# Optimization experiments

Hardware: AMD Instinct MI355X
Metric: run time of the kernel (lower is better)

The kernel has to match this reference:

```python
import jax, jax.numpy as jnp
import numpy as np

B, S_X, S_Y = 2, 2048, 2048
C1, C2, H, D, W_EXP = 1024, 1024, 16, 64, 4
EPS = 1e-5


def _layernorm(x, w, b):
    mu = jnp.mean(x, axis=-1, keepdims=True)
    var = jnp.mean(jnp.square(x - mu), axis=-1, keepdims=True)
    return (x - mu) * jax.lax.rsqrt(var + EPS) * w + b


def setup_inputs() -> dict:
    key = jax.random.key(0)
    ks = jax.random.split(key, 12)
    s = lambda fan_in: 1.0 / np.sqrt(fan_in)
    inp = {
        "x": jax.random.normal(ks[0], (B, S_X, C1), jnp.float32),
        "y": jax.random.normal(ks[1], (B, S_Y, C2), jnp.float32),
        # per-head projections, batched over heads: [H, in, d]
        "Wq": jax.random.uniform(ks[2], (H, C1, D), jnp.float32, -s(C1), s(C1)),
        "Wk": jax.random.uniform(ks[3], (H, C2, D), jnp.float32, -s(C2), s(C2)),
        "Wv": jax.random.uniform(ks[4], (H, C2, D), jnp.float32, -s(C2), s(C2)),
        "li1_w": jax.random.uniform(ks[5], (H * D, C1), jnp.float32, -s(H * D), s(H * D)),
        "li1_b": jax.random.uniform(ks[6], (C1,), jnp.float32, -s(H * D), s(H * D)),
        "ln1_w": jnp.ones((C1,), jnp.float32),
        "ln1_b": jnp.zeros((C1,), jnp.float32),
        "ln2_w": jnp.ones((C2,), jnp.float32),
        "ln2_b": jnp.zeros((C2,), jnp.float32),
        "ln3_w": jnp.ones((C1,), jnp.float32),
        "ln3_b": jnp.zeros((C1,), jnp.float32),
        "li2_w": jax.random.uniform(ks[7], (C1, C1 * W_EXP), jnp.float32, -s(C1), s(C1)),
        "li2_b": jax.random.uniform(ks[8], (C1 * W_EXP,), jnp.float32, -s(C1), s(C1)),
        "li3_w": jax.random.uniform(ks[9], (C1 * W_EXP, C1), jnp.float32, -s(C1 * W_EXP), s(C1 * W_EXP)),
        "li3_b": jax.random.uniform(ks[10], (C1,), jnp.float32, -s(C1 * W_EXP), s(C1 * W_EXP)),
    }
    return inp


def reference(x, y, Wq, Wk, Wv, li1_w, li1_b, ln1_w, ln1_b, ln2_w, ln2_b,
              ln3_w, ln3_b, li2_w, li2_b, li3_w, li3_b):
    xn = _layernorm(x, ln1_w, ln1_b)            # [B, Sx, C1]
    yn = _layernorm(y, ln2_w, ln2_b)            # [B, Sy, C2]
    # batched per-head projections (original loops over 16 Head modules)
    q = jnp.einsum("bsc,hcd->bhsd", xn, Wq)
    k = jnp.einsum("btc,hcd->bhtd", yn, Wk)
    v = jnp.einsum("btc,hcd->bhtd", yn, Wv)
    a = jnp.einsum("bhsd,bhtd->bhst", q, k) * (D ** -0.5)
    a = jax.nn.softmax(a, axis=-1)
    # faithful to original: triu(diagonal=1) applied AFTER softmax (zeros diag too)
    mask = jnp.triu(jnp.ones((S_X, S_Y), bool), k=1)
    a = jnp.where(mask, a, 0.0)
    o = jnp.einsum("bhst,bhtd->bhsd", a, v)     # [B, H, Sx, D]
    o = o.transpose(0, 2, 1, 3).reshape(B, S_X, H * D)  # concat heads
    x_out = x + o @ li1_w + li1_b
    h = _layernorm(x_out, ln3_w, ln3_b)
    h = jax.nn.gelu(h @ li2_w + li2_b, approximate=False)
    h = h @ li3_w + li3_b
    return x_out + h
```

## Files before the change

### kernel.cpp

```cpp
#include <hip/hip_runtime.h>
#include <hip/hip_bf16.h>


typedef __hip_bfloat16 bf16;
typedef __attribute__((ext_vector_type(8))) short  s16x8;
typedef __attribute__((ext_vector_type(4))) short  s16x4;
typedef __attribute__((ext_vector_type(4))) float  f32x4;
typedef __attribute__((ext_vector_type(4))) _Float16 h16x4;

__device__ __forceinline__ float bfbits2f(short s) {
    return __uint_as_float(((unsigned)(unsigned short)s) << 16);
}
__device__ __forceinline__ float load_in(const void* p, size_t i, int f32) {
    return f32 ? ((const float*)p)[i] : bfbits2f(((const short*)p)[i]);
}
__device__ __forceinline__ void async16(const short* g, short* l) {
    __builtin_amdgcn_global_load_lds(
        (const __attribute__((address_space(1))) void*)g,
        (__attribute__((address_space(3))) void*)l, 16, 0, 0);
}
__device__ __forceinline__ float gelu_fast(float x) {
    float x2 = x * x;
    float z  = x * (0.7978845608f + 0.0356774081f * x2);
    z = fminf(z, 15.f);
    float e  = __expf(2.f * z);
    float t  = (e - 1.f) * __builtin_amdgcn_rcpf(e + 1.f);
    return 0.5f * x * (1.f + t);
}

__global__ __launch_bounds__(256)
void detect_dtype(const short* __restrict__ x, int* __restrict__ flag)
{
    const int tid = threadIdx.x;
    int cnt = 0;
#pragma unroll
    for (int e = 0; e < 16; e++) {
        int idx = (tid * 16 + e) * 2;
        int ex  = (x[idx] >> 7) & 0xFF;
        if (ex >= 113 && ex <= 142) cnt++;
    }
#pragma unroll
    for (int off = 1; off < 64; off <<= 1) cnt += __shfl_xor(cnt, off, 64);
    __shared__ int sh[4];
    if ((tid & 63) == 0) sh[tid >> 6] = cnt;
    __syncthreads();
    if (tid == 0) {
        int tot = sh[0] + sh[1] + sh[2] + sh[3];
        flag[0] = (tot < 2458) ? 1 : 0;
    }
}

__global__ __launch_bounds__(256)
void conv_bias3(const void* b1, const void* b2, const void* b3,
                bf16* o1, bf16* o2, bf16* o3, const int* __restrict__ flag)
{
    const int f32 = flag[0];
    int i = blockIdx.x * 256 + threadIdx.x;
    if (i < 1024)      o1[i]        = __float2bfloat16(load_in(b1, i, f32));
    else if (i < 5120) o2[i - 1024] = __float2bfloat16(load_in(b2, i - 1024, f32));
    else               o3[i - 5120] = __float2bfloat16(load_in(b3, i - 5120, f32));
}

__global__ __launch_bounds__(256)
void transpose_tiled(const void* __restrict__ in, bf16* __restrict__ out,
                     int R, int Cc, const int* __restrict__ flag)
{
    __shared__ float tile[32][33];
    const int f32 = flag[0];
    const int tx = threadIdx.x & 31, ty = threadIdx.x >> 5;
    const int c0 = blockIdx.x * 32, r0 = blockIdx.y * 32;
#pragma unroll
    for (int i = 0; i < 4; i++)
        tile[ty + i * 8][tx] = load_in(in, (size_t)(r0 + ty + i * 8) * Cc + c0 + tx, f32);
    __syncthreads();
#pragma unroll
    for (int i = 0; i < 4; i++)
        out[(size_t)(c0 + ty + i * 8) * R + r0 + tx] = __float2bfloat16(tile[tx][ty + i * 8]);
}

__global__ __launch_bounds__(256)
void pack_qkv_tiled(const void* __restrict__ in, bf16* __restrict__ out,
                    const int* __restrict__ flag)
{
    __shared__ float tile[32][33];
    const int f32 = flag[0];
    const int tx = threadIdx.x & 31, ty = threadIdx.x >> 5;
    const int c0 = blockIdx.x * 32, r0 = blockIdx.y * 32;
    const size_t base = (size_t)blockIdx.z * 1024 * 64;
#pragma unroll
    for (int i = 0; i < 4; i++)
        tile[ty + i * 8][tx] = load_in(in, base + (size_t)(r0 + ty + i * 8) * 64 + c0 + tx, f32);
    __syncthreads();
#pragma unroll
    for (int i = 0; i < 4; i++)
        out[base + (size_t)(c0 + ty + i * 8) * 1024 + r0 + tx] =
            __float2bfloat16(tile[tx][ty + i * 8]);
}

__global__ __launch_bounds__(256)
void v_transpose(const bf16* __restrict__ KV, _Float16* __restrict__ Vt)
{
    __shared__ short tile[32][33];
    const int tx = threadIdx.x & 31, ty = threadIdx.x >> 5;
    const int t0 = blockIdx.x * 32, hd0 = blockIdx.y * 32, b = blockIdx.z;
#pragma unroll
    for (int i = 0; i < 4; i++)
        tile[ty + i * 8][tx] =
            ((const short*)KV)[(size_t)(b * 2048 + t0 + ty + i * 8) * 2048 + 1024 + hd0 + tx];
    __syncthreads();
#pragma unroll
    for (int i = 0; i < 4; i++)
        Vt[(size_t)(b * 1024 + hd0 + ty + i * 8) * 2048 + t0 + tx] =
            (_Float16)bfbits2f(tile[tx][ty + i * 8]);
}

__global__ __launch_bounds__(256)
void ln_kernel(const void* __restrict__ x, const void* __restrict__ w,
               const void* __restrict__ bv, bf16* __restrict__ out,
               const int* __restrict__ flag, int x_is_bf16,
               bf16* __restrict__ copy_out)
{
    const int f32  = flag[0];
    const int xf32 = x_is_bf16 ? 0 : f32;
    const int row  = blockIdx.x;
    const int tid  = threadIdx.x;
    const int lane = tid & 63;
    const int wave = tid >> 6;
    const size_t base = (size_t)row * 1024 + tid * 4;

    float v[4];
    float sum = 0.f, ss = 0.f;
#pragma unroll
    for (int e = 0; e < 4; e++) {
        v[e] = load_in(x, base + e, xf32);
        sum += v[e]; ss += v[e] * v[e];
    }
    if (copy_out) {
        s16x4 c;
#pragma unroll
        for (int e = 0; e < 4; e++) {
            __hip_bfloat16 hb = __float2bfloat16(v[e]);
            c[e] = *(short*)&hb;
        }
        *(s16x4*)((short*)copy_out + base) = c;
    }
#pragma unroll
    for (int off = 1; off < 64; off <<= 1) {
        sum += __shfl_xor(sum, off, 64);
        ss  += __shfl_xor(ss,  off, 64);
    }
    __shared__ float sh1[4], sh2[4];
    if (lane == 0) { sh1[wave] = sum; sh2[wave] = ss; }
    __syncthreads();
    float t1 = sh1[0] + sh1[1] + sh1[2] + sh1[3];
    float t2 = sh2[0] + sh2[1] + sh2[2] + sh2[3];
    float mu   = t1 * (1.f / 1024.f);
    float var  = t2 * (1.f / 1024.f) - mu * mu;
    float rstd = rsqrtf(var + 1e-5f);

#pragma unroll
    for (int e = 0; e < 4; e++) {
        float ov = (v[e] - mu) * rstd * load_in(w, tid * 4 + e, f32)
                 + load_in(bv, tid * 4 + e, f32);
        out[base + e] = __float2bfloat16(ov);
    }
}

template<int KU>
__global__ __launch_bounds__(256)
void gemm_bt64(const bf16* __restrict__ A, const bf16* __restrict__ Bt,
               const bf16* __restrict__ bias, const bf16* __restrict__ res,
               void* __restrict__ C, int M, int N, int K, int act,
               const int* __restrict__ dflag, int final_out, float ascale)
{
    __shared__ alignas(16) short As[KU][128][64];
    __shared__ alignas(16) short Bs[KU][64][64];

    const int f32out = final_out ? dflag[0] : 0;
    const int tid  = threadIdx.x;
    const int lane = tid & 63;
    const int wave = tid >> 6;
    const int q    = lane >> 4;
    const int l15  = lane & 15;
    const int wm   = (wave >> 1) * 64;
    const int wn   = (wave & 1) * 32;
    const int bm   = blockIdx.x * 128;
    const int bn   = blockIdx.y * 64;

    const int srow   = lane >> 3;
    const int gchunk = (lane & 7) ^ srow;
    const short* Ab = (const short*)A  + (size_t)(bm + wave * 32 + srow) * K + gchunk * 8;
    const short* Bb = (const short*)Bt + (size_t)(bn + wave * 16 + srow) * K + gchunk * 8;
    const int csw = l15 & 7;

    f32x4 acc[4][2] = {};

    for (int k0 = 0; k0 < K; k0 += 64 * KU) {
        __syncthreads();
#pragma unroll
        for (int u = 0; u < KU; u++) {
            const int ko = k0 + u * 64;
            async16(Ab + ko,                  &As[u][wave * 32][0]);
            async16(Ab + ko + (size_t)8  * K, &As[u][wave * 32 + 8][0]);
            async16(Ab + ko + (size_t)16 * K, &As[u][wave * 32 + 16][0]);
            async16(Ab + ko + (size_t)24 * K, &As[u][wave * 32 + 24][0]);
            async16(Bb + ko,                  &Bs[u][wave * 16][0]);
            async16(Bb + ko + (size_t)8  * K, &Bs[u][wave * 16 + 8][0]);
        }
        __syncthreads();

#pragma unroll
        for (int u = 0; u < KU; u++) {
            s16x8 af[4][2], bfr[2][2];
#pragma unroll
            for (int i = 0; i < 4; i++)
#pragma unroll
                for (int kk = 0; kk < 2; kk++)
                    af[i][kk] = *(const s16x8*)&As[u][wm + i * 16 + l15][((kk * 4 + q) ^ csw) * 8];
#pragma unroll
            for (int j = 0; j < 2; j++)
#pragma unroll
                for (int kk = 0; kk < 2; kk++)
                    bfr[j][kk] = *(const s16x8*)&Bs[u][wn + j * 16 + l15][((kk * 4 + q) ^ csw) * 8];
#pragma unroll
            for (int i = 0; i < 4; i++)
#pragma unroll
                for (int j = 0; j < 2; j++) {
                    acc[i][j] = __builtin_amdgcn_mfma_f32_16x16x32_bf16(af[i][0], bfr[j][0], acc[i][j], 0, 0, 0);
                    acc[i][j] = __builtin_amdgcn_mfma_f32_16x16x32_bf16(af[i][1], bfr[j][1], acc[i][j], 0, 0, 0);
                }
        }
    }

#pragma unroll
    for (int i = 0; i < 4; i++) {
#pragma unroll
        for (int j = 0; j < 2; j++) {
            int n = bn + wn + j * 16 + l15;
            float bvv = bias ? __bfloat162float(bias[n]) : 0.f;
#pragma unroll
            for (int r = 0; r < 4; r++) {
                int m = bm + wm + i * 16 + q * 4 + r;
                float v = acc[i][j][r] * ascale + bvv;
                if (act) v = gelu_fast(v);
                if (res) v += __bfloat162float(res[(size_t)m * N + n]);
                size_t idx = (size_t)m * N + n;
                if (f32out) ((float*)C)[idx] = v;
                else        ((bf16*)C)[idx]  = __float2bfloat16(v);
            }
        }
    }
}

__global__ __launch_bounds__(256)
void gemm_bt128(const bf16* __restrict__ A, const bf16* __restrict__ Bt,
                const bf16* __restrict__ bias, const bf16* __restrict__ res,
                void* __restrict__ C, int M, int N, int K, int act,
                const int* __restrict__ dflag, int final_out)
{
    __shared__ alignas(16) short As[128][64];
    __shared__ alignas(16) short Bs[128][64];

    const int f32out = final_out ? dflag[0] : 0;
    const int tid  = threadIdx.x;
    const int lane = tid & 63;
    const int wave = tid >> 6;
    const int q    = lane >> 4;
    const int l15  = lane & 15;
    const int wm   = (wave >> 1) * 64;
    const int wn   = (wave & 1) * 64;
    const int bm   = blockIdx.x * 128;
    const int bn   = blockIdx.y * 128;

    const int srow   = lane >> 3;
    const int gchunk = (lane & 7) ^ srow;
    const short* Ab = (const short*)A  + (size_t)(bm + wave * 32 + srow) * K + gchunk * 8;
    const short* Bb = (const short*)Bt + (size_t)(bn + wave * 32 + srow) * K + gchunk * 8;
    const int csw = l15 & 7;

    f32x4 acc[4][4] = {};

    for (int k0 = 0; k0 < K; k0 += 64) {
        __syncthreads();
#pragma unroll
        for (int r8 = 0; r8 < 4; r8++) {
            async16(Ab + k0 + (size_t)(r8 * 8) * K, &As[wave * 32 + r8 * 8][0]);
            async16(Bb + k0 + (size_t)(r8 * 8) * K, &Bs[wave * 32 + r8 * 8][0]);
        }
        __syncthreads();

#pragma unroll
        for (int kk = 0; kk < 2; kk++) {
            s16x8 af[4], bfr[4];
#pragma unroll
            for (int i = 0; i < 4; i++) af[i]  = *(const s16x8*)&As[wm + i * 16 + l15][((kk * 4 + q) ^ csw) * 8];
#pragma unroll
            for (int j = 0; j < 4; j++) bfr[j] = *(const s16x8*)&Bs[wn + j * 16 + l15][((kk * 4 + q) ^ csw) * 8];
#pragma unroll
            for (int i = 0; i < 4; i++)
#pragma unroll
                for (int j = 0; j < 4; j++)
                    acc[i][j] = __builtin_amdgcn_mfma_f32_16x16x32_bf16(af[i], bfr[j], acc[i][j], 0, 0, 0);
        }
    }

#pragma unroll
    for (int i = 0; i < 4; i++) {
#pragma unroll
        for (int j = 0; j < 4; j++) {
            int n = bn + wn + j * 16 + l15;
            float bvv = bias ? __bfloat162float(bias[n]) : 0.f;
#pragma unroll
            for (int r = 0; r < 4; r++) {
                int m = bm + wm + i * 16 + q * 4 + r;
                float v = acc[i][j][r] + bvv;
                if (act) v = gelu_fast(v);
                if (res) v += __bfloat162float(res[(size_t)m * N + n]);
                size_t idx = (size_t)m * N + n;
                if (f32out) ((float*)C)[idx] = v;
                else        ((bf16*)C)[idx]  = __float2bfloat16(v);
            }
        }
    }
}

__global__ __launch_bounds__(256)
void attn_kernel(const bf16* __restrict__ Q, const bf16* __restrict__ KV,
                 const _Float16* __restrict__ Vt, bf16* __restrict__ O)
{
    __shared__ alignas(16) short    Ks[64][64];
    __shared__ alignas(16) _Float16 Vs[64][64];

    const int tid  = threadIdx.x;
    const int lane = tid & 63;
    const int wave = tid >> 6;
    const int q    = lane >> 4;
    const int l15  = lane & 15;
    const int bh   = blockIdx.x;
    const int b    = bh >> 4, h = bh & 15;
    const int sblk   = blockIdx.y * 64;
    const int s_base = sblk + wave * 16;
    const int s_glob = s_base + l15;

    const short* qrow = (const short*)Q + (size_t)(b * 2048 + s_glob) * 1024 + h * 64;
    s16x8 qf0 = *(const s16x8*)(qrow + q * 8);
    s16x8 qf1 = *(const s16x8*)(qrow + 32 + q * 8);

    float l_lane = 0.f;
    f32x4 o_acc[4] = {};

    const int srow = lane >> 3;
    const int gch  = (lane & 7) ^ srow;
    const short*    kbase = (const short*)KV +
        (size_t)(b * 2048 + wave * 16 + srow) * 2048 + h * 64 + gch * 8;
    const _Float16* vbase = Vt +
        (size_t)(b * 1024 + h * 64 + wave * 16 + srow) * 2048 + gch * 8;
    const int key = l15 & 7;

    for (int t0 = 0; t0 < 2048; t0 += 64) {
        const bool needV = (t0 >= sblk);
        const short*    kg = kbase + (size_t)t0 * 2048;
        const _Float16* vg = vbase + t0;
        __syncthreads();
        async16(kg,                    &Ks[wave * 16][0]);
        async16(kg + (size_t)8 * 2048, &Ks[wave * 16 + 8][0]);
        if (needV) {
            async16((const short*)vg,                      (short*)&Vs[wave * 16][0]);
            async16((const short*)(vg + (size_t)8 * 2048), (short*)&Vs[wave * 16 + 8][0]);
        }
        __syncthreads();

#pragma unroll
        for (int sub = 0; sub < 4; sub++) {
            const int tb  = sub * 16;
            const int rel = t0 + tb - s_base;
            s16x8 kf0 = *(const s16x8*)&Ks[tb + l15][(q ^ key) * 8];
            s16x8 kf1 = *(const s16x8*)&Ks[tb + l15][((q + 4) ^ key) * 8];
            f32x4 st = {};
            st = __builtin_amdgcn_mfma_f32_16x16x32_bf16(kf0, qf0, st, 0, 0, 0);
            st = __builtin_amdgcn_mfma_f32_16x16x32_bf16(kf1, qf1, st, 0, 0, 0);
            float p[4];
#pragma unroll
            for (int r = 0; r < 4; r++) {
                p[r] = __expf(st[r]);
                l_lane += p[r];
            }
            if (rel >= 0) {
                h16x4 pf;
                if (rel == 0) {
#pragma unroll
                    for (int r = 0; r < 4; r++)
                        pf[r] = (q * 4 + r > l15) ? (_Float16)p[r] : (_Float16)0.f;
                } else {
#pragma unroll
                    for (int r = 0; r < 4; r++) pf[r] = (_Float16)p[r];
                }
#pragma unroll
                for (int dt = 0; dt < 4; dt++) {
                    h16x4 vf = *(const h16x4*)&Vs[dt * 16 + l15]
                        [(((2 * sub + (q >> 1)) ^ key) * 8) + (q & 1) * 4];
                    o_acc[dt] = __builtin_amdgcn_mfma_f32_16x16x16f16(pf, vf, o_acc[dt], 0, 0, 0);
                }
            }
        }
    }

    float l = l_lane;
    l += __shfl_xor(l, 16, 64);
    l += __shfl_xor(l, 32, 64);
    float linv[4];
#pragma unroll
    for (int r = 0; r < 4; r++) linv[r] = 1.f / __shfl(l, q * 4 + r, 64);
#pragma unroll
    for (int dt = 0; dt < 4; dt++)
#pragma unroll
        for (int r = 0; r < 4; r++) {
            int s = s_base + q * 4 + r;
            int d = dt * 16 + l15;
            O[(size_t)(b * 2048 + s) * 1024 + h * 64 + d] =
                __float2bfloat16(o_acc[dt][r] * linv[r]);
        }
}

extern "C" void kernel_launch(void* const* d_in, const int* in_sizes, int n_in,
                              void* d_out, int out_size, void* d_ws, size_t ws_size,
                              hipStream_t stream)
{
    const void* x     = d_in[0];
    const void* y     = d_in[1];
    const void* Wq    = d_in[2];
    const void* Wk    = d_in[3];
    const void* Wv    = d_in[4];
    const void* li1_w = d_in[5];
    const void* li1_b = d_in[6];
    const void* ln1_w = d_in[7];
    const void* ln1_b = d_in[8];
    const void* ln2_w = d_in[9];
    const void* ln2_b = d_in[10];
    const void* ln3_w = d_in[11];
    const void* ln3_b = d_in[12];
    const void* li2_w = d_in[13];
    const void* li2_b = d_in[14];
    const void* li3_w = d_in[15];
    const void* li3_b = d_in[16];

    char* w = (char*)d_ws;
    const size_t MB = 1u << 20;
    bf16* xn    = (bf16*)(w + 0 * MB);
    bf16* yn    = (bf16*)(w + 8 * MB);
    bf16* WqT   = (bf16*)(w + 16 * MB);
    bf16* WkT   = (bf16*)(w + 18 * MB);
    bf16* WvT   = (bf16*)(w + 20 * MB);
    bf16* li1T  = (bf16*)(w + 22 * MB);
    bf16* li2T  = (bf16*)(w + 24 * MB);
    bf16* li3T  = (bf16*)(w + 32 * MB);
    bf16* xout  = (bf16*)(w + 40 * MB);
    bf16* Qb    = (bf16*)(w + 48 * MB);
    bf16* KVb   = (bf16*)(w + 56 * MB);
    _Float16* Vt = (_Float16*)(w + 72 * MB);
    bf16* h2    = (bf16*)(w + 48 * MB);
    bf16* xc    = (bf16*)(w + 80 * MB);
    int*  flag  = (int*) (w + 88 * MB);
    bf16* li1bc = (bf16*)(w + 88 * MB + 4096);
    bf16* li2bc = (bf16*)(w + 88 * MB + 8192);
    bf16* li3bc = (bf16*)(w + 88 * MB + 24576);
    bf16* Ob    = yn;
    bf16* hn    = xn;

    detect_dtype<<<1, 256, 0, stream>>>((const short*)x, flag);

    conv_bias3<<<24, 256, 0, stream>>>(li1_b, li2_b, li3_b, li1bc, li2bc, li3bc, flag);

    ln_kernel<<<4096, 256, 0, stream>>>(x, ln1_w, ln1_b, xn, flag, 0, xc);
    ln_kernel<<<4096, 256, 0, stream>>>(y, ln2_w, ln2_b, yn, flag, 0, nullptr);

    pack_qkv_tiled<<<dim3(2, 32, 16), 256, 0, stream>>>(Wq, WqT, flag);
    pack_qkv_tiled<<<dim3(2, 32, 16), 256, 0, stream>>>(Wk, WkT, flag);
    pack_qkv_tiled<<<dim3(2, 32, 16), 256, 0, stream>>>(Wv, WvT, flag);
    transpose_tiled<<<dim3(32, 32),  256, 0, stream>>>(li1_w, li1T, 1024, 1024, flag);
    transpose_tiled<<<dim3(128, 32), 256, 0, stream>>>(li2_w, li2T, 1024, 4096, flag);
    transpose_tiled<<<dim3(32, 128), 256, 0, stream>>>(li3_w, li3T, 4096, 1024, flag);

    gemm_bt64<2><<<dim3(32, 16), 256, 0, stream>>>(xn, WqT, nullptr, nullptr, Qb, 4096, 1024, 1024, 0, flag, 0, 0.125f);
    gemm_bt64<1><<<dim3(32, 32), 256, 0, stream>>>(yn, WkT, nullptr, nullptr, KVb, 4096, 2048, 1024, 0, flag, 0, 1.0f);
    v_transpose<<<dim3(64, 32, 2), 256, 0, stream>>>(KVb, Vt);

    attn_kernel<<<dim3(32, 32), 256, 0, stream>>>(Qb, KVb, Vt, Ob);

    gemm_bt64<2><<<dim3(32, 16), 256, 0, stream>>>(Ob, li1T, li1bc, xc, xout, 4096, 1024, 1024, 0, flag, 0, 1.0f);

    ln_kernel<<<4096, 256, 0, stream>>>(xout, ln3_w, ln3_b, hn, flag, 1, nullptr);

    gemm_bt128<<<dim3(32, 32), 256, 0, stream>>>(hn, li2T, li2bc, nullptr, h2, 4096, 4096, 1024, 1, flag, 0);

    gemm_bt64<2><<<dim3(32, 16), 256, 0, stream>>>(h2, li3T, li3bc, xout, d_out, 4096, 1024, 4096, 0, flag, 1, 1.0f);
}
```

Baseline: 447.8 us.

## Load two 64-key tiles per barrier in attention; use exact erf GELU

The attention kernel now stages 128 keys per iteration into two LDS buffers, which halves the number of barrier pairs and issues more async loads before each wait. It also replaces the tanh-approximation GELU in the GEMM epilogues with the exact erf form. The erf form matches the reference's approximate=False but costs more per element. Doubling the LDS tiles may reduce occupancy.

```diff
diff --git a/kernel.cpp b/kernel.cpp
--- a/kernel.cpp
+++ b/kernel.cpp
@@ -18,14 +18,6 @@
     __builtin_amdgcn_global_load_lds(
         (const __attribute__((address_space(1))) void*)g,
         (__attribute__((address_space(3))) void*)l, 16, 0, 0);
-}
-__device__ __forceinline__ float gelu_fast(float x) {
-    float x2 = x * x;
-    float z  = x * (0.7978845608f + 0.0356774081f * x2);
-    z = fminf(z, 15.f);
-    float e  = __expf(2.f * z);
-    float t  = (e - 1.f) * __builtin_amdgcn_rcpf(e + 1.f);
-    return 0.5f * x * (1.f + t);
 }
 
 __global__ __launch_bounds__(256)
@@ -242,7 +234,7 @@
             for (int r = 0; r < 4; r++) {
                 int m = bm + wm + i * 16 + q * 4 + r;
                 float v = acc[i][j][r] * ascale + bvv;
-                if (act) v = gelu_fast(v);
+                if (act) v = 0.5f * v * (1.f + erff(v * 0.70710678118f));
                 if (res) v += __bfloat162float(res[(size_t)m * N + n]);
                 size_t idx = (size_t)m * N + n;
                 if (f32out) ((float*)C)[idx] = v;
@@ -314,7 +306,7 @@
             for (int r = 0; r < 4; r++) {
                 int m = bm + wm + i * 16 + q * 4 + r;
                 float v = acc[i][j][r] + bvv;
-                if (act) v = gelu_fast(v);
+                if (act) v = 0.5f * v * (1.f + erff(v * 0.70710678118f));
                 if (res) v += __bfloat162float(res[(size_t)m * N + n]);
                 size_t idx = (size_t)m * N + n;
                 if (f32out) ((float*)C)[idx] = v;
@@ -328,8 +320,8 @@
 void attn_kernel(const bf16* __restrict__ Q, const bf16* __restrict__ KV,
                  const _Float16* __restrict__ Vt, bf16* __restrict__ O)
 {
-    __shared__ alignas(16) short    Ks[64][64];
-    __shared__ alignas(16) _Float16 Vs[64][64];
+    __shared__ alignas(16) short    Ks[2][64][64];
+    __shared__ alignas(16) _Float16 Vs[2][64][64];
 
     const int tid  = threadIdx.x;
     const int lane = tid & 63;
@@ -357,49 +349,55 @@
         (size_t)(b * 1024 + h * 64 + wave * 16 + srow) * 2048 + gch * 8;
     const int key = l15 & 7;
 
-    for (int t0 = 0; t0 < 2048; t0 += 64) {
-        const bool needV = (t0 >= sblk);
-        const short*    kg = kbase + (size_t)t0 * 2048;
-        const _Float16* vg = vbase + t0;
-        __syncthreads();
-        async16(kg,                    &Ks[wave * 16][0]);
-        async16(kg + (size_t)8 * 2048, &Ks[wave * 16 + 8][0]);
-        if (needV) {
-            async16((const short*)vg,                      (short*)&Vs[wave * 16][0]);
-            async16((const short*)(vg + (size_t)8 * 2048), (short*)&Vs[wave * 16 + 8][0]);
-        }
-        __syncthreads();
-
-#pragma unroll
-        for (int sub = 0; sub < 4; sub++) {
-            const int tb  = sub * 16;
-            const int rel = t0 + tb - s_base;
-            s16x8 kf0 = *(const s16x8*)&Ks[tb + l15][(q ^ key) * 8];
-            s16x8 kf1 = *(const s16x8*)&Ks[tb + l15][((q + 4) ^ key) * 8];
-            f32x4 st = {};
-            st = __builtin_amdgcn_mfma_f32_16x16x32_bf16(kf0, qf0, st, 0, 0, 0);
-            st = __builtin_amdgcn_mfma_f32_16x16x32_bf16(kf1, qf1, st, 0, 0, 0);
-            float p[4];
-#pragma unroll
-            for (int r = 0; r < 4; r++) {
-                p[r] = __expf(st[r]);
-                l_lane += p[r];
+    for (int t0 = 0; t0 < 2048; t0 += 128) {
+        __syncthreads();
+#pragma unroll
+        for (int u = 0; u < 2; u++) {
+            const int tt = t0 + u * 64;
+            const short* kg = kbase + (size_t)tt * 2048;
+            async16(kg,                    &Ks[u][wave * 16][0]);
+            async16(kg + (size_t)8 * 2048, &Ks[u][wave * 16 + 8][0]);
+            if (tt >= sblk) {
+                const _Float16* vg = vbase + tt;
+                async16((const short*)vg,                      (short*)&Vs[u][wave * 16][0]);
+                async16((const short*)(vg + (size_t)8 * 2048), (short*)&Vs[u][wave * 16 + 8][0]);
             }
-            if (rel >= 0) {
-                h16x4 pf;
-                if (rel == 0) {
-#pragma unroll
-                    for (int r = 0; r < 4; r++)
-                        pf[r] = (q * 4 + r > l15) ? (_Float16)p[r] : (_Float16)0.f;
-                } else {
-#pragma unroll
-                    for (int r = 0; r < 4; r++) pf[r] = (_Float16)p[r];
+        }
+        __syncthreads();
+
+#pragma unroll
+        for (int u = 0; u < 2; u++) {
+#pragma unroll
+            for (int sub = 0; sub < 4; sub++) {
+                const int tb  = sub * 16;
+                const int rel = t0 + u * 64 + tb - s_base;
+                s16x8 kf0 = *(const s16x8*)&Ks[u][tb + l15][(q ^ key) * 8];
+                s16x8 kf1 = *(const s16x8*)&Ks[u][tb + l15][((q + 4) ^ key) * 8];
+                f32x4 st = {};
+                st = __builtin_amdgcn_mfma_f32_16x16x32_bf16(kf0, qf0, st, 0, 0, 0);
+                st = __builtin_amdgcn_mfma_f32_16x16x32_bf16(kf1, qf1, st, 0, 0, 0);
+                float p[4];
+#pragma unroll
+                for (int r = 0; r < 4; r++) {
+                    p[r] = __expf(st[r]);
+                    l_lane += p[r];
                 }
-#pragma unroll
-                for (int dt = 0; dt < 4; dt++) {
-                    h16x4 vf = *(const h16x4*)&Vs[dt * 16 + l15]
-                        [(((2 * sub + (q >> 1)) ^ key) * 8) + (q & 1) * 4];
-                    o_acc[dt] = __builtin_amdgcn_mfma_f32_16x16x16f16(pf, vf, o_acc[dt], 0, 0, 0);
+                if (rel >= 0) {
+                    h16x4 pf;
+                    if (rel == 0) {
+#pragma unroll
+                        for (int r = 0; r < 4; r++)
+                            pf[r] = (q * 4 + r > l15) ? (_Float16)p[r] : (_Float16)0.f;
+                    } else {
+#pragma unroll
+                        for (int r = 0; r < 4; r++) pf[r] = (_Float16)p[r];
+                    }
+#pragma unroll
+                    for (int dt = 0; dt < 4; dt++) {
+                        h16x4 vf = *(const h16x4*)&Vs[u][dt * 16 + l15]
+                            [(((2 * sub + (q >> 1)) ^ key) * 8) + (q & 1) * 4];
+                        o_acc[dt] = __builtin_amdgcn_mfma_f32_16x16x16f16(pf, vf, o_acc[dt], 0, 0, 0);
+                    }
                 }
             }
         }
```

New measurement: 483.8 us. +8.0%, slower.
